# Kernel tuning notes

Measured on AMD Instinct MI355X. Metric: run time of the kernel, lower is better.

## Reference

```python
import jax, jax.numpy as jnp
import numpy as np

N = 100000   # nodes
E = 1600000  # edges
D = 128      # input feature dim
H = 128      # hidden dim
C = 10       # output classes
G = 64       # graphs in batch


def setup_inputs() -> dict:
    key = jax.random.key(0)
    ks = jax.random.split(key, 24)
    s = 0.02
    lin = lambda k, i, o: jax.random.normal(k, (i, o), jnp.float32) * s
    inp = {
        'x': jax.random.normal(ks[0], (N, D), jnp.float32),
        'edge_index': jax.random.randint(ks[1], (2, E), 0, N),
        'batch': jnp.sort(jax.random.randint(ks[2], (N,), 0, G)),
        # GIN conv 0: Linear(D,H)-ReLU-Linear(H,H)
        'w1_0': lin(ks[3], D, H), 'b1_0': jnp.zeros((H,), jnp.float32),
        'w2_0': lin(ks[4], H, H), 'b2_0': jnp.zeros((H,), jnp.float32),
        # GIN conv 1
        'w1_1': lin(ks[5], H, H), 'b1_1': jnp.zeros((H,), jnp.float32),
        'w2_1': lin(ks[6], H, H), 'b2_1': jnp.zeros((H,), jnp.float32),
        # GIN conv 2
        'w1_2': lin(ks[7], H, H), 'b1_2': jnp.zeros((H,), jnp.float32),
        'w2_2': lin(ks[8], H, H), 'b2_2': jnp.zeros((H,), jnp.float32),
        # LayerNorms (applied after layers 0 and 1)
        'ln_g0': jnp.ones((H,), jnp.float32), 'ln_b0': jnp.zeros((H,), jnp.float32),
        'ln_g1': jnp.ones((H,), jnp.float32), 'ln_b1': jnp.zeros((H,), jnp.float32),
        # post_mp: Linear(H,H) -> Dropout -> Linear(H,C)
        'pw1': lin(ks[9], H, H), 'pb1': jnp.zeros((H,), jnp.float32),
        'pw2': lin(ks[10], H, C), 'pb2': jnp.zeros((C,), jnp.float32),
    }
    return inp


def _gin_conv(x, src, dst, w1, b1, w2, b2):
    # GINConv with eps=0: MLP(x + sum_{j->i} x_j)
    agg = jax.ops.segment_sum(x[src], dst, num_segments=N)  # [N, d]
    h = x + agg
    h = jax.nn.relu(h @ w1 + b1) @ w2 + b2
    return h


def _layernorm(x, g, b, eps=1e-5):
    mu = jnp.mean(x, axis=-1, keepdims=True)
    var = jnp.var(x, axis=-1, keepdims=True)
    return (x - mu) * jax.lax.rsqrt(var + eps) * g + b


def reference(x, edge_index, batch,
              w1_0, b1_0, w2_0, b2_0,
              w1_1, b1_1, w2_1, b2_1,
              w1_2, b1_2, w2_2, b2_2,
              ln_g0, ln_b0, ln_g1, ln_b1,
              pw1, pb1, pw2, pb2):
    src, dst = edge_index[0], edge_index[1]
    convs = [(w1_0, b1_0, w2_0, b2_0), (w1_1, b1_1, w2_1, b2_1), (w1_2, b1_2, w2_2, b2_2)]
    lns = [(ln_g0, ln_b0), (ln_g1, ln_b1)]
    emb = x
    h = x
    for i in range(3):
        w1, b1, w2, b2 = convs[i]
        h = _gin_conv(h, src, dst, w1, b1, w2, b2)
        emb = h
        h = jax.nn.relu(h)
        # dropout p=0.25: identity in eval mode
        if i != 2:
            g, b = lns[i]
            h = _layernorm(h, g, b)
    # global mean pool over graphs
    sums = jax.ops.segment_sum(h, batch, num_segments=G)          # [G, H]
    cnts = jax.ops.segment_sum(jnp.ones((N,), h.dtype), batch, num_segments=G)
    pooled = sums / jnp.maximum(cnts, 1.0)[:, None]
    # post_mp (dropout identity in eval)
    z = pooled @ pw1 + pb1
    logits = z @ pw2 + pb2
    return emb, jax.nn.log_softmax(logits, axis=1)
```

## Files before the change

### kernel.cpp

```cpp
#include <hip/hip_runtime.h>

typedef __bf16 bf16_t;
typedef __bf16 bf16x8 __attribute__((ext_vector_type(8)));
typedef float floatx4 __attribute__((ext_vector_type(4)));

constexpr int N = 100000;
constexpr int E = 1600000;
constexpr int H = 128;
constexpr int G = 64;
constexpr int C = 10;
constexpr int NBLK = (N + 255) / 256;

constexpr int FPART = 8;
constexpr int FPART_SZ = (N + FPART - 1) / FPART;
constexpr int BCHUNK = 1024;
constexpr int BBLK = (E + BCHUNK - 1) / BCHUNK;
constexpr int BCAP = 204800;

__device__ inline float bflo(unsigned u) {
  return __builtin_bit_cast(float, u << 16);
}
__device__ inline float bfhi(unsigned u) {
  return __builtin_bit_cast(float, u & 0xffff0000u);
}
__device__ inline unsigned short f2b(float f) {
  return __builtin_bit_cast(unsigned short, (bf16_t)f);
}
__device__ inline unsigned pack2(float a, float b) {
  return (unsigned)f2b(a) | ((unsigned)f2b(b) << 16);
}

__global__ __launch_bounds__(256) void tobf_kernel(const float* __restrict__ x,
                                                   uint4* __restrict__ xb) {
  const int g = blockIdx.x * 256 + threadIdx.x;
  const float4 a = *(const float4*)(x + (size_t)g * 8);
  const float4 b = *(const float4*)(x + (size_t)g * 8 + 4);
  uint4 o;
  o.x = pack2(a.x, a.y);
  o.y = pack2(a.z, a.w);
  o.z = pack2(b.x, b.y);
  o.w = pack2(b.z, b.w);
  xb[g] = o;
}

__global__ __launch_bounds__(256) void bucket_kernel(
    const int* __restrict__ src, const int* __restrict__ dst,
    int* __restrict__ deg, unsigned* __restrict__ buckets,
    int* __restrict__ bcnt) {
  __shared__ int offS[4][FPART];
  __shared__ int waveExcl[4][FPART];
  __shared__ int cntA[FPART];
  __shared__ int baseS[FPART];
  const int tid = threadIdx.x;
  const int wave = tid >> 6;
  const int lane = tid & 63;
  if (tid < 32) ((int*)offS)[tid] = 0;
  __syncthreads();

  const int e0 = blockIdx.x * BCHUNK + tid * 4;
  int d[4], s[4];
  int nv = 0;
  if (e0 + 4 <= E) {
    const int4 d4 = *(const int4*)(dst + e0);
    const int4 s4 = *(const int4*)(src + e0);
    d[0] = d4.x; d[1] = d4.y; d[2] = d4.z; d[3] = d4.w;
    s[0] = s4.x; s[1] = s4.y; s[2] = s4.z; s[3] = s4.w;
    nv = 4;
  } else {
    nv = (e0 < E) ? (E - e0) : 0;
    for (int j = 0; j < nv; ++j) {
      d[j] = dst[e0 + j];
      s[j] = src[e0 + j];
    }
    for (int j = nv; j < 4; ++j) { d[j] = 0; s[j] = 0; }
  }

  const unsigned long long below = (lane == 63)
      ? 0xFFFFFFFFFFFFFFFFull >> 1
      : ((1ull << lane) - 1ull);

  int pj[4];
  int slotW[4];

#pragma unroll
  for (int j = 0; j < 4; ++j) {
    const bool valid = (j < nv);
    if (valid) atomicAdd(&deg[d[j]], 1);
    const int p = d[j] / FPART_SZ;
    pj[j] = p;
    unsigned long long mown = 0;
#pragma unroll
    for (int q = 0; q < FPART; ++q) {
      const unsigned long long mq = __ballot(valid && (p == q));
      if (p == q) mown = mq;
    }
    const int cnt = (int)__popcll(mown);
    const int rank = (int)__popcll(mown & below);
    const int base = offS[wave][p];
    if (valid && rank == 0) offS[wave][p] = base + cnt;
    slotW[j] = base + rank;
  }
  __syncthreads();

  if (tid < FPART) {
    int running = 0;
#pragma unroll
    for (int w = 0; w < 4; ++w) {
      waveExcl[w][tid] = running;
      running += offS[w][tid];
    }
    cntA[tid] = running;
  }
  __syncthreads();
  if (tid < FPART) baseS[tid] = atomicAdd(&bcnt[tid], cntA[tid]);
  __syncthreads();

#pragma unroll
  for (int j = 0; j < 4; ++j) {
    if (j < nv) {
      const int p = pj[j];
      const int g = baseS[p] + waveExcl[wave][p] + slotW[j];
      buckets[p * BCAP + g] =
          ((unsigned)s[j] << 14) | (unsigned)(d[j] - p * FPART_SZ);
    }
  }
}

__global__ __launch_bounds__(256) void partial_kernel(
    const int* __restrict__ deg, int* __restrict__ partials) {
  __shared__ int sm[256];
  const int tid = threadIdx.x;
  const int i = blockIdx.x * 256 + tid;
  sm[tid] = (i < N) ? deg[i] : 0;
  __syncthreads();
  for (int off = 128; off > 0; off >>= 1) {
    if (tid < off) sm[tid] += sm[tid + off];
    __syncthreads();
  }
  if (tid == 0) partials[blockIdx.x] = sm[0];
}

__global__ __launch_bounds__(512) void scanp_kernel(
    const int* __restrict__ partials, int* __restrict__ blockbase) {
  __shared__ int p[512];
  const int t = threadIdx.x;
  p[t] = (t < NBLK) ? partials[t] : 0;
  __syncthreads();
  for (int off = 1; off < 512; off <<= 1) {
    int v = 0;
    if (t >= off) v = p[t - off];
    __syncthreads();
    p[t] += v;
    __syncthreads();
  }
  if (t < NBLK) blockbase[t] = (t == 0) ? 0 : p[t - 1];
}

__global__ __launch_bounds__(256) void expand_kernel(
    const int* __restrict__ deg, const int* __restrict__ blockbase,
    int* __restrict__ rowptr, int* __restrict__ cursor) {
  __shared__ int sm[256];
  const int tid = threadIdx.x;
  const int i = blockIdx.x * 256 + tid;
  const int d = (i < N) ? deg[i] : 0;
  sm[tid] = d;
  __syncthreads();
  for (int off = 1; off < 256; off <<= 1) {
    int v = 0;
    if (tid >= off) v = sm[tid - off];
    __syncthreads();
    sm[tid] += v;
    __syncthreads();
  }
  const int excl = sm[tid] - d + blockbase[blockIdx.x];
  if (i < N) {
    rowptr[i] = excl;
    cursor[i] = excl;
  }
  if (i == N - 1) rowptr[N] = excl + d;
}

__global__ __launch_bounds__(256) void fill2_kernel(
    const unsigned* __restrict__ buckets, const int* __restrict__ bcnt,
    int* __restrict__ cursor, int* __restrict__ csr_src) {
  const int part = blockIdx.x & (FPART - 1);
  const int blk = blockIdx.x >> 3;
  const int nblk = gridDim.x >> 3;
  const int cnt = bcnt[part];
  const unsigned* b = buckets + part * BCAP;
  const int dbase = part * FPART_SZ;
  for (int i = blk * 256 + threadIdx.x; i < cnt; i += nblk * 256) {
    const unsigned u = b[i];
    const int d = dbase + (int)(u & 0x3FFFu);
    const int s = (int)(u >> 14);
    const int slot = atomicAdd(&cursor[d], 1);
    csr_src[slot] = s;
  }
}

__global__ __launch_bounds__(256) void gather_kernel(
    const uint4* __restrict__ h, const int* __restrict__ rowptr,
    const int* __restrict__ csr_src, uint4* __restrict__ pre) {
  const int node = blockIdx.x * 16 + (threadIdx.x >> 4);
  const int l = threadIdx.x & 15;
  const int r0 = rowptr[node];
  const int r1 = rowptr[node + 1];
  const uint4 v = h[(size_t)node * 16 + l];
  float a0 = bflo(v.x), a1 = bfhi(v.x), a2 = bflo(v.y), a3 = bfhi(v.y);
  float a4 = bflo(v.z), a5 = bfhi(v.z), a6 = bflo(v.w), a7 = bfhi(v.w);
  int s = r0;
  for (; s + 3 < r1; s += 4) {
    const int i0 = csr_src[s], i1 = csr_src[s + 1];
    const int i2 = csr_src[s + 2], i3 = csr_src[s + 3];
    const uint4 u0 = h[(size_t)i0 * 16 + l];
    const uint4 u1 = h[(size_t)i1 * 16 + l];
    const uint4 u2 = h[(size_t)i2 * 16 + l];
    const uint4 u3 = h[(size_t)i3 * 16 + l];
    a0 += bflo(u0.x); a1 += bfhi(u0.x); a2 += bflo(u0.y); a3 += bfhi(u0.y);
    a4 += bflo(u0.z); a5 += bfhi(u0.z); a6 += bflo(u0.w); a7 += bfhi(u0.w);
    a0 += bflo(u1.x); a1 += bfhi(u1.x); a2 += bflo(u1.y); a3 += bfhi(u1.y);
    a4 += bflo(u1.z); a5 += bfhi(u1.z); a6 += bflo(u1.w); a7 += bfhi(u1.w);
    a0 += bflo(u2.x); a1 += bfhi(u2.x); a2 += bflo(u2.y); a3 += bfhi(u2.y);
    a4 += bflo(u2.z); a5 += bfhi(u2.z); a6 += bflo(u2.w); a7 += bfhi(u2.w);
    a0 += bflo(u3.x); a1 += bfhi(u3.x); a2 += bflo(u3.y); a3 += bfhi(u3.y);
    a4 += bflo(u3.z); a5 += bfhi(u3.z); a6 += bflo(u3.w); a7 += bfhi(u3.w);
  }
  for (; s < r1; ++s) {
    const uint4 u = h[(size_t)csr_src[s] * 16 + l];
    a0 += bflo(u.x); a1 += bfhi(u.x); a2 += bflo(u.y); a3 += bfhi(u.y);
    a4 += bflo(u.z); a5 += bfhi(u.z); a6 += bflo(u.w); a7 += bfhi(u.w);
  }
  uint4 o;
  o.x = pack2(a0, a1);
  o.y = pack2(a2, a3);
  o.z = pack2(a4, a5);
  o.w = pack2(a6, a7);
  pre[(size_t)node * 16 + l] = o;
}

template <int MODE>
__global__ __launch_bounds__(256) void mlp_kernel(
    const unsigned short* __restrict__ pre_g,
    const float* __restrict__ w1, const float* __restrict__ b1,
    const float* __restrict__ w2, const float* __restrict__ b2,
    const float* __restrict__ lng, const float* __restrict__ lnb,
    unsigned short* __restrict__ h_out,
    float* __restrict__ emb) {
  __shared__ unsigned short preS[32 * 136];
  __shared__ unsigned short hidS[32 * 136];
  __shared__ float muS[32];
  __shared__ float rsS[32];

  const int tid = threadIdx.x;
  const int wave = tid >> 6;
  const int lane = tid & 63;
  const int quad = lane >> 4;
  const int l16 = lane & 15;

  union F8 { bf16x8 v; bf16_t e[8]; };

  bf16x8 w1f[4][2], w2f[4][2];
#pragma unroll
  for (int nn = 0; nn < 2; ++nn) {
    const int col = wave * 32 + nn * 16 + l16;
#pragma unroll
    for (int kt = 0; kt < 4; ++kt) {
      F8 t1, t2;
#pragma unroll
      for (int j = 0; j < 8; ++j) {
        const int k = kt * 32 + quad * 8 + j;
        t1.e[j] = (bf16_t)w1[k * H + col];
        t2.e[j] = (bf16_t)w2[k * H + col];
      }
      w1f[kt][nn] = t1.v;
      w2f[kt][nn] = t2.v;
    }
  }
  const float b1v[2] = {b1[wave * 32 + l16], b1[wave * 32 + 16 + l16]};
  const float b2v[2] = {b2[wave * 32 + l16], b2[wave * 32 + 16 + l16]};
  float lng0 = 0.f, lng1 = 0.f, lnb0 = 0.f, lnb1 = 0.f;
  const int c2 = (tid * 2) & 127;
  if (MODE == 0) {
    lng0 = lng[c2]; lng1 = lng[c2 + 1];
    lnb0 = lnb[c2]; lnb1 = lnb[c2 + 1];
  }

  for (int tile = blockIdx.x; tile < N / 32; tile += gridDim.x) {
    const size_t base = (size_t)tile * 32 * H;
    {
      const uint4* srcp = (const uint4*)(pre_g + base);
#pragma unroll
      for (int it = 0; it < 2; ++it) {
        const int chunk = it * 256 + tid;
        const int row = chunk >> 4;
        const int colc = (chunk & 15) * 8;
        *(uint4*)&preS[row * 136 + colc] = srcp[chunk];
      }
    }
    __syncthreads();

    {
      floatx4 acc[2][2];
#pragma unroll
      for (int i = 0; i < 2; ++i)
#pragma unroll
        for (int j = 0; j < 2; ++j) acc[i][j] = {0.f, 0.f, 0.f, 0.f};
#pragma unroll
      for (int kt = 0; kt < 4; ++kt) {
        const int kc = kt * 32 + quad * 8;
        const bf16x8 a0 =
            __builtin_bit_cast(bf16x8, *(const uint4*)&preS[l16 * 136 + kc]);
        const bf16x8 a1 = __builtin_bit_cast(
            bf16x8, *(const uint4*)&preS[(16 + l16) * 136 + kc]);
        acc[0][0] = __builtin_amdgcn_mfma_f32_16x16x32_bf16(a0, w1f[kt][0],
                                                            acc[0][0], 0, 0, 0);
        acc[0][1] = __builtin_amdgcn_mfma_f32_16x16x32_bf16(a0, w1f[kt][1],
                                                            acc[0][1], 0, 0, 0);
        acc[1][0] = __builtin_amdgcn_mfma_f32_16x16x32_bf16(a1, w1f[kt][0],
                                                            acc[1][0], 0, 0, 0);
        acc[1][1] = __builtin_amdgcn_mfma_f32_16x16x32_bf16(a1, w1f[kt][1],
                                                            acc[1][1], 0, 0, 0);
      }
#pragma unroll
      for (int mt = 0; mt < 2; ++mt)
#pragma unroll
        for (int nn = 0; nn < 2; ++nn) {
          const int col = wave * 32 + nn * 16 + l16;
#pragma unroll
          for (int r = 0; r < 4; ++r) {
            const int row = mt * 16 + quad * 4 + r;
            const float v = fmaxf(acc[mt][nn][r] + b1v[nn], 0.f);
            hidS[row * 136 + col] = f2b(v);
          }
        }
    }
    __syncthreads();

    {
      floatx4 acc[2][2];
#pragma unroll
      for (int i = 0; i < 2; ++i)
#pragma unroll
        for (int j = 0; j < 2; ++j) acc[i][j] = {0.f, 0.f, 0.f, 0.f};
#pragma unroll
      for (int kt = 0; kt < 4; ++kt) {
        const int kc = kt * 32 + quad * 8;
        const bf16x8 a0 =
            __builtin_bit_cast(bf16x8, *(const uint4*)&hidS[l16 * 136 + kc]);
        const bf16x8 a1 = __builtin_bit_cast(
            bf16x8, *(const uint4*)&hidS[(16 + l16) * 136 + kc]);
        acc[0][0] = __builtin_amdgcn_mfma_f32_16x16x32_bf16(a0, w2f[kt][0],
                                                            acc[0][0], 0, 0, 0);
        acc[0][1] = __builtin_amdgcn_mfma_f32_16x16x32_bf16(a0, w2f[kt][1],
                                                            acc[0][1], 0, 0, 0);
        acc[1][0] = __builtin_amdgcn_mfma_f32_16x16x32_bf16(a1, w2f[kt][0],
                                                            acc[1][0], 0, 0, 0);
        acc[1][1] = __builtin_amdgcn_mfma_f32_16x16x32_bf16(a1, w2f[kt][1],
                                                            acc[1][1], 0, 0, 0);
      }
#pragma unroll
      for (int mt = 0; mt < 2; ++mt)
#pragma unroll
        for (int nn = 0; nn < 2; ++nn) {
          const int col = wave * 32 + nn * 16 + l16;
#pragma unroll
          for (int r = 0; r < 4; ++r) {
            const int row = mt * 16 + quad * 4 + r;
            float v = acc[mt][nn][r] + b2v[nn];
            if (MODE == 0) v = fmaxf(v, 0.f);
            preS[row * 136 + col] = f2b(v);
          }
        }
    }
    __syncthreads();

    if (MODE == 0) {
      const int n = tid >> 3;
      const int j = tid & 7;
      float s = 0.f, sq = 0.f;
#pragma unroll
      for (int t = 0; t < 16; ++t) {
        const float v =
            __builtin_bit_cast(float, (unsigned)preS[n * 136 + j + 8 * t] << 16);
        s += v;
        sq += v * v;
      }
      s += __shfl_xor(s, 1); sq += __shfl_xor(sq, 1);
      s += __shfl_xor(s, 2); sq += __shfl_xor(sq, 2);
      s += __shfl_xor(s, 4); sq += __shfl_xor(sq, 4);
      if (j == 0) {
        const float mu = s * (1.f / H);
        const float var = sq * (1.f / H) - mu * mu;
        muS[n] = mu;
        rsS[n] = rsqrtf(var + 1e-5f);
      }
      __syncthreads();
      unsigned* ho = (unsigned*)(h_out + base);
#pragma unroll
      for (int it = 0; it < 8; ++it) {
        const int idx = it * 512 + tid * 2;
        const int row = idx >> 7;
        const int k = idx & 127;
        const unsigned pr = *(const unsigned*)&preS[row * 136 + k];
        const float mu = muS[row], rs = rsS[row];
        const float v0 = (bflo(pr) - mu) * rs * lng0 + lnb0;
        const float v1 = (bfhi(pr) - mu) * rs * lng1 + lnb1;
        ho[idx >> 1] = pack2(v0, v1);
      }
    } else {
      unsigned* ho = (unsigned*)(h_out + base);
#pragma unroll
      for (int it = 0; it < 8; ++it) {
        const int idx = it * 512 + tid * 2;
        const int row = idx >> 7;
        const int k = idx & 127;
        const unsigned pr = *(const unsigned*)&preS[row * 136 + k];
        const float v0 = bflo(pr);
        const float v1 = bfhi(pr);
        *(float2*)&emb[base + idx] = make_float2(v0, v1);
        ho[idx >> 1] = pack2(fmaxf(v0, 0.f), fmaxf(v1, 0.f));
      }
    }
    __syncthreads();
  }
}

__global__ __launch_bounds__(256) void pool_kernel(
    const uint4* __restrict__ hv, const int* __restrict__ batch,
    float* __restrict__ pooled, float* __restrict__ cnt) {
  __shared__ int bs[256];
  __shared__ float smr[512];
  __shared__ int endS;
  const int tid = threadIdx.x;
  const int c0 = blockIdx.x * 256;
  const int len = min(256, N - c0);
  if (tid < len) bs[tid] = batch[c0 + tid];
  __syncthreads();

  const int nl = tid >> 4;
  const int fg = tid & 15;
  const int wave = tid >> 6;
  const int lane = tid & 63;

  int start = 0;
  while (start < len) {
    const int g = bs[start];
    if (tid == 0) endS = len;
    __syncthreads();
    for (int i = start + tid; i < len; i += 256)
      if (bs[i] != g) atomicMin(&endS, i);
    __syncthreads();
    const int end = endS;

    float a0 = 0.f, a1 = 0.f, a2 = 0.f, a3 = 0.f;
    float a4 = 0.f, a5 = 0.f, a6 = 0.f, a7 = 0.f;
    for (int i = start + nl; i < end; i += 16) {
      const uint4 u = hv[(size_t)(c0 + i) * 16 + fg];
      a0 += bflo(u.x); a1 += bfhi(u.x); a2 += bflo(u.y); a3 += bfhi(u.y);
      a4 += bflo(u.z); a5 += bfhi(u.z); a6 += bflo(u.w); a7 += bfhi(u.w);
    }
    a0 += __shfl_xor(a0, 16); a1 += __shfl_xor(a1, 16);
    a2 += __shfl_xor(a2, 16); a3 += __shfl_xor(a3, 16);
    a4 += __shfl_xor(a4, 16); a5 += __shfl_xor(a5, 16);
    a6 += __shfl_xor(a6, 16); a7 += __shfl_xor(a7, 16);
    a0 += __shfl_xor(a0, 32); a1 += __shfl_xor(a1, 32);
    a2 += __shfl_xor(a2, 32); a3 += __shfl_xor(a3, 32);
    a4 += __shfl_xor(a4, 32); a5 += __shfl_xor(a5, 32);
    a6 += __shfl_xor(a6, 32); a7 += __shfl_xor(a7, 32);
    if (lane < 16) {
      float* d = &smr[wave * 128 + lane * 8];
      d[0] = a0; d[1] = a1; d[2] = a2; d[3] = a3;
      d[4] = a4; d[5] = a5; d[6] = a6; d[7] = a7;
    }
    __syncthreads();
    if (tid < 128) {
      const float s =
          smr[tid] + smr[128 + tid] + smr[256 + tid] + smr[384 + tid];
      atomicAdd(&pooled[g * H + tid], s);
    }
    if (tid == 0) atomicAdd(&cnt[g], (float)(end - start));
    __syncthreads();
    start = end;
  }
}

__global__ __launch_bounds__(128) void head_kernel(
    const float* __restrict__ pooled, const float* __restrict__ cnt,
    const float* __restrict__ pw1, const float* __restrict__ pb1,
    const float* __restrict__ pw2, const float* __restrict__ pb2,
    float* __restrict__ out_logp) {
  __shared__ float p[H];
  __shared__ float z[H];
  __shared__ float l[C];
  const int g = blockIdx.x;
  const int f = threadIdx.x;
  const float c = fmaxf(cnt[g], 1.f);
  p[f] = pooled[g * H + f] / c;
  __syncthreads();
  float a = pb1[f];
  for (int k = 0; k < H; ++k) a += p[k] * pw1[k * H + f];
  z[f] = a;
  __syncthreads();
  if (f < C) {
    float a2 = pb2[f];
    for (int k = 0; k < H; ++k) a2 += z[k] * pw2[k * C + f];
    l[f] = a2;
  }
  __syncthreads();
  if (f == 0) {
    float m = l[0];
    for (int i = 1; i < C; ++i) m = fmaxf(m, l[i]);
    float s = 0.f;
    for (int i = 0; i < C; ++i) s += expf(l[i] - m);
    const float lse = m + logf(s);
    for (int i = 0; i < C; ++i) out_logp[g * C + i] = l[i] - lse;
  }
}

extern "C" void kernel_launch(void* const* d_in, const int* in_sizes, int n_in,
                              void* d_out, int out_size, void* d_ws,
                              size_t ws_size, hipStream_t stream) {
  const float* x = (const float*)d_in[0];
  const int* ei = (const int*)d_in[1];
  const int* src = ei;
  const int* dst = ei + E;
  const int* batch = (const int*)d_in[2];
  const float* w1_0 = (const float*)d_in[3];
  const float* b1_0 = (const float*)d_in[4];
  const float* w2_0 = (const float*)d_in[5];
  const float* b2_0 = (const float*)d_in[6];
  const float* w1_1 = (const float*)d_in[7];
  const float* b1_1 = (const float*)d_in[8];
  const float* w2_1 = (const float*)d_in[9];
  const float* b2_1 = (const float*)d_in[10];
  const float* w1_2 = (const float*)d_in[11];
  const float* b1_2 = (const float*)d_in[12];
  const float* w2_2 = (const float*)d_in[13];
  const float* b2_2 = (const float*)d_in[14];
  const float* ln_g0 = (const float*)d_in[15];
  const float* ln_b0 = (const float*)d_in[16];
  const float* ln_g1 = (const float*)d_in[17];
  const float* ln_b1 = (const float*)d_in[18];
  const float* pw1 = (const float*)d_in[19];
  const float* pb1 = (const float*)d_in[20];
  const float* pw2 = (const float*)d_in[21];
  const float* pb2 = (const float*)d_in[22];

  unsigned short* xb = (unsigned short*)d_ws;
  unsigned short* hb = xb + (size_t)N * H;
  unsigned short* pre = hb + (size_t)N * H;
  float* pooled = (float*)(pre + (size_t)N * H);
  float* cnt = pooled + (size_t)G * H;
  int* deg = (int*)(cnt + G);
  int* rowptr = deg + N;
  int* cursor = rowptr + N + 1;
  int* csr_src = cursor + N;
  int* partials = csr_src + E;
  int* blockbase = partials + NBLK;
  int* bcnt = blockbase + NBLK;
  unsigned* buckets = (unsigned*)pre;
  float* emb = (float*)d_out;
  float* logp = emb + (size_t)N * H;

  tobf_kernel<<<N * H / (256 * 8), 256, 0, stream>>>(x, (uint4*)xb);

  hipMemsetAsync(deg, 0, (size_t)N * sizeof(int), stream);
  hipMemsetAsync(bcnt, 0, (size_t)FPART * sizeof(int), stream);
  bucket_kernel<<<BBLK, 256, 0, stream>>>(src, dst, deg, buckets, bcnt);
  partial_kernel<<<NBLK, 256, 0, stream>>>(deg, partials);
  scanp_kernel<<<1, 512, 0, stream>>>(partials, blockbase);
  expand_kernel<<<NBLK, 256, 0, stream>>>(deg, blockbase, rowptr, cursor);
  fill2_kernel<<<2048, 256, 0, stream>>>(buckets, bcnt, cursor, csr_src);

  gather_kernel<<<N / 16, 256, 0, stream>>>((const uint4*)xb, rowptr, csr_src,
                                            (uint4*)pre);
  mlp_kernel<0><<<2048, 256, 0, stream>>>(pre, w1_0, b1_0, w2_0, b2_0, ln_g0,
                                          ln_b0, hb, nullptr);
  gather_kernel<<<N / 16, 256, 0, stream>>>((const uint4*)hb, rowptr, csr_src,
                                            (uint4*)pre);
  mlp_kernel<0><<<2048, 256, 0, stream>>>(pre, w1_1, b1_1, w2_1, b2_1, ln_g1,
                                          ln_b1, hb, nullptr);
  gather_kernel<<<N / 16, 256, 0, stream>>>((const uint4*)hb, rowptr, csr_src,
                                            (uint4*)pre);
  mlp_kernel<1><<<2048, 256, 0, stream>>>(pre, w1_2, b1_2, w2_2, b2_2, nullptr,
                                          nullptr, hb, emb);

  hipMemsetAsync(pooled, 0, (size_t)(G * H + G) * sizeof(float), stream);
  pool_kernel<<<NBLK, 256, 0, stream>>>((const uint4*)hb, batch, pooled, cnt);
  head_kernel<<<G, 128, 0, stream>>>(pooled, cnt, pw1, pb1, pw2, pb2, logp);
}
```

Baseline: 583.3 us.

## Stage bucket writes in LDS and compute degrees via shared-memory histogram

The bucket kernel now handles 8 edges per thread (2048 per block) and stages its bucketed entries in LDS, so each partition is written to global memory as one contiguous run instead of as scattered stores. The per-edge global atomicAdd on the degree array is removed. A new deghist kernel instead builds per-partition degree histograms in shared memory from the buckets and flushes them with one atomic per nonzero node. This trades random global atomics for an extra pass over the bucket data and an additional kernel launch.

```diff
diff --git a/kernel.cpp b/kernel.cpp
--- a/kernel.cpp
+++ b/kernel.cpp
@@ -13,7 +13,7 @@
 
 constexpr int FPART = 8;
 constexpr int FPART_SZ = (N + FPART - 1) / FPART;
-constexpr int BCHUNK = 1024;
+constexpr int BCHUNK = 2048;
 constexpr int BBLK = (E + BCHUNK - 1) / BCHUNK;
 constexpr int BCAP = 204800;
 
@@ -45,47 +45,50 @@
 
 __global__ __launch_bounds__(256) void bucket_kernel(
     const int* __restrict__ src, const int* __restrict__ dst,
-    int* __restrict__ deg, unsigned* __restrict__ buckets,
-    int* __restrict__ bcnt) {
+    unsigned* __restrict__ buckets, int* __restrict__ bcnt) {
   __shared__ int offS[4][FPART];
   __shared__ int waveExcl[4][FPART];
   __shared__ int cntA[FPART];
+  __shared__ int blockExcl[FPART];
   __shared__ int baseS[FPART];
+  __shared__ unsigned stage[BCHUNK];
   const int tid = threadIdx.x;
   const int wave = tid >> 6;
   const int lane = tid & 63;
   if (tid < 32) ((int*)offS)[tid] = 0;
   __syncthreads();
 
-  const int e0 = blockIdx.x * BCHUNK + tid * 4;
-  int d[4], s[4];
+  const int e0 = blockIdx.x * BCHUNK + tid * 8;
+  int d[8], s[8];
   int nv = 0;
-  if (e0 + 4 <= E) {
-    const int4 d4 = *(const int4*)(dst + e0);
-    const int4 s4 = *(const int4*)(src + e0);
-    d[0] = d4.x; d[1] = d4.y; d[2] = d4.z; d[3] = d4.w;
-    s[0] = s4.x; s[1] = s4.y; s[2] = s4.z; s[3] = s4.w;
-    nv = 4;
+  if (e0 + 8 <= E) {
+    const int4 da = *(const int4*)(dst + e0);
+    const int4 db = *(const int4*)(dst + e0 + 4);
+    const int4 sa = *(const int4*)(src + e0);
+    const int4 sb = *(const int4*)(src + e0 + 4);
+    d[0] = da.x; d[1] = da.y; d[2] = da.z; d[3] = da.w;
+    d[4] = db.x; d[5] = db.y; d[6] = db.z; d[7] = db.w;
+    s[0] = sa.x; s[1] = sa.y; s[2] = sa.z; s[3] = sa.w;
+    s[4] = sb.x; s[5] = sb.y; s[6] = sb.z; s[7] = sb.w;
+    nv = 8;
   } else {
     nv = (e0 < E) ? (E - e0) : 0;
+    if (nv > 8) nv = 8;
     for (int j = 0; j < nv; ++j) {
       d[j] = dst[e0 + j];
       s[j] = src[e0 + j];
     }
-    for (int j = nv; j < 4; ++j) { d[j] = 0; s[j] = 0; }
-  }
-
-  const unsigned long long below = (lane == 63)
-      ? 0xFFFFFFFFFFFFFFFFull >> 1
-      : ((1ull << lane) - 1ull);
-
-  int pj[4];
-  int slotW[4];
-
-#pragma unroll
-  for (int j = 0; j < 4; ++j) {
+    for (int j = nv; j < 8; ++j) { d[j] = 0; s[j] = 0; }
+  }
+
+  const unsigned long long below = (1ull << lane) - 1ull;
+
+  int pj[8];
+  int slotW[8];
+
+#pragma unroll
+  for (int j = 0; j < 8; ++j) {
     const bool valid = (j < nv);
-    if (valid) atomicAdd(&deg[d[j]], 1);
     const int p = d[j] / FPART_SZ;
     pj[j] = p;
     unsigned long long mown = 0;
@@ -110,19 +113,55 @@
       running += offS[w][tid];
     }
     cntA[tid] = running;
-  }
-  __syncthreads();
-  if (tid < FPART) baseS[tid] = atomicAdd(&bcnt[tid], cntA[tid]);
-  __syncthreads();
-
-#pragma unroll
-  for (int j = 0; j < 4; ++j) {
+    baseS[tid] = atomicAdd(&bcnt[tid], running);
+  }
+  __syncthreads();
+  if (tid < FPART) {
+    int ex = 0;
+    for (int q = 0; q < tid; ++q) ex += cntA[q];
+    blockExcl[tid] = ex;
+  }
+  __syncthreads();
+
+#pragma unroll
+  for (int j = 0; j < 8; ++j) {
     if (j < nv) {
       const int p = pj[j];
-      const int g = baseS[p] + waveExcl[wave][p] + slotW[j];
-      buckets[p * BCAP + g] =
+      stage[blockExcl[p] + waveExcl[wave][p] + slotW[j]] =
           ((unsigned)s[j] << 14) | (unsigned)(d[j] - p * FPART_SZ);
     }
+  }
+  __syncthreads();
+
+#pragma unroll
+  for (int p = 0; p < FPART; ++p) {
+    const int c = cntA[p];
+    const int gb = p * BCAP + baseS[p];
+    const int lb = blockExcl[p];
+    for (int i = tid; i < c; i += 256) buckets[gb + i] = stage[lb + i];
+  }
+}
+
+__global__ __launch_bounds__(256) void deghist_kernel(
+    const unsigned* __restrict__ buckets, const int* __restrict__ bcnt,
+    int* __restrict__ deg) {
+  __shared__ int cntS[FPART_SZ];
+  const int part = blockIdx.x & (FPART - 1);
+  const int sub = blockIdx.x >> 3;
+  for (int i = threadIdx.x; i < FPART_SZ; i += 256) cntS[i] = 0;
+  __syncthreads();
+  const int cnt = bcnt[part];
+  const int per = (cnt + 7) >> 3;
+  const int lo = sub * per;
+  const int hi = min(lo + per, cnt);
+  const unsigned* b = buckets + part * BCAP;
+  for (int i = lo + threadIdx.x; i < hi; i += 256)
+    atomicAdd(&cntS[b[i] & 0x3FFFu], 1);
+  __syncthreads();
+  const int dbase = part * FPART_SZ;
+  for (int i = threadIdx.x; i < FPART_SZ; i += 256) {
+    const int c = cntS[i];
+    if (c) atomicAdd(&deg[dbase + i], c);
   }
 }
 
@@ -566,7 +605,8 @@
 
   hipMemsetAsync(deg, 0, (size_t)N * sizeof(int), stream);
   hipMemsetAsync(bcnt, 0, (size_t)FPART * sizeof(int), stream);
-  bucket_kernel<<<BBLK, 256, 0, stream>>>(src, dst, deg, buckets, bcnt);
+  bucket_kernel<<<BBLK, 256, 0, stream>>>(src, dst, buckets, bcnt);
+  deghist_kernel<<<64, 256, 0, stream>>>(buckets, bcnt, deg);
   partial_kernel<<<NBLK, 256, 0, stream>>>(deg, partials);
   scanp_kernel<<<1, 512, 0, stream>>>(partials, blockbase);
   expand_kernel<<<NBLK, 256, 0, stream>>>(deg, blockbase, rowptr, cursor);
```

New measurement: 551.4 us. 1.06x faster.
